# Kernel optimization log

Measured on AMD Instinct MI355X. Metric: run time of the kernel, lower is better.

The kernel has to match this reference:

```python
import jax, jax.numpy as jnp
import numpy as np

N = 50000
IN_C = 128
HID = 64
HEADS = 4
OUT_C = 64
E_RAND = 800000
NEG_SLOPE = 0.2  # PyG GATConv default


def setup_inputs() -> dict:
    key = jax.random.key(0)
    ks = jax.random.split(key, 10)
    x = jax.random.normal(ks[0], (N, IN_C), dtype=jnp.float32)
    src = jax.random.randint(ks[1], (E_RAND,), 0, N)
    dst = jax.random.randint(ks[2], (E_RAND,), 0, N)
    loops = jnp.arange(N)
    # PyG GATConv adds self-loops by default; append them here
    edge_index = jnp.stack([jnp.concatenate([src, loops]),
                            jnp.concatenate([dst, loops])], axis=0).astype(jnp.int64)
    s = 0.05
    W1 = jax.random.normal(ks[3], (IN_C, HEADS * HID), dtype=jnp.float32) * s
    att_src1 = jax.random.normal(ks[4], (HEADS, HID), dtype=jnp.float32) * s
    att_dst1 = jax.random.normal(ks[5], (HEADS, HID), dtype=jnp.float32) * s
    b1 = jnp.zeros((HEADS * HID,), dtype=jnp.float32)
    W2 = jax.random.normal(ks[6], (HEADS * HID, OUT_C), dtype=jnp.float32) * s
    att_src2 = jax.random.normal(ks[7], (1, OUT_C), dtype=jnp.float32) * s
    att_dst2 = jax.random.normal(ks[8], (1, OUT_C), dtype=jnp.float32) * s
    b2 = jnp.zeros((OUT_C,), dtype=jnp.float32)
    return {"x": x, "edge_index": edge_index, "W1": W1, "att_src1": att_src1,
            "att_dst1": att_dst1, "b1": b1, "W2": W2, "att_src2": att_src2,
            "att_dst2": att_dst2, "b2": b2}


def gat_conv(x, src, dst, W, att_src, att_dst, bias, heads, ch, concat):
    n = x.shape[0]
    h = (x @ W).reshape(n, heads, ch)                      # [N,H,C]
    a_src = jnp.einsum('nhc,hc->nh', h, att_src)           # [N,H]
    a_dst = jnp.einsum('nhc,hc->nh', h, att_dst)
    e = jax.nn.leaky_relu(a_src[src] + a_dst[dst], NEG_SLOPE)  # [E,H]
    # segment softmax over incoming edges of each dst node
    m = jax.ops.segment_max(e, dst, num_segments=n)
    ex = jnp.exp(e - m[dst])
    ssum = jax.ops.segment_sum(ex, dst, num_segments=n)
    alpha = ex / jnp.where(ssum[dst] > 0, ssum[dst], 1.0)  # [E,H]
    msg = h[src] * alpha[:, :, None]                        # [E,H,C]
    out = jax.ops.segment_sum(msg, dst, num_segments=n)     # [N,H,C]
    out = out.reshape(n, heads * ch) if concat else out.mean(axis=1)
    return out + bias


def reference(x, edge_index, W1, att_src1, att_dst1, b1, W2, att_src2, att_dst2, b2):
    src, dst = edge_index[0], edge_index[1]
    # eval mode: feature dropout and attention dropout are identity
    h = gat_conv(x, src, dst, W1, att_src1, att_dst1, b1, HEADS, HID, True)
    h = jax.nn.elu(h)
    out = gat_conv(h, src, dst, W2, att_src2, att_dst2, b2, 1, OUT_C, False)
    return out
```

## Files before the change

kernel.cpp:

```cpp
#include <hip/hip_runtime.h>
#include <hip/hip_bf16.h>

#define IN_C 128
#define HID 64
#define HEADS 4
#define OUT_C 64
#define NEG_SLOPE 0.2f

typedef __attribute__((ext_vector_type(8))) short bfrag8;
typedef __attribute__((ext_vector_type(4))) float facc4;

__device__ __forceinline__ float bf16u_to_f(unsigned short u) {
  return __uint_as_float(((unsigned)u) << 16);
}
__device__ __forceinline__ float lof(unsigned u) {
  return __uint_as_float(u << 16);
}
__device__ __forceinline__ float hif(unsigned u) {
  return __uint_as_float(u & 0xffff0000u);
}
__device__ __forceinline__ unsigned short f_to_bf16u(float f) {
  return __bfloat16_as_ushort(__float2bfloat16(f));
}
__device__ __forceinline__ float leaky(float x) {
  return (x > 0.f) ? x : NEG_SLOPE * x;
}

__global__ __launch_bounds__(256) void cvt_w_kernel(
    const float* __restrict__ W1, const float* __restrict__ W2,
    unsigned short* __restrict__ B1img, unsigned short* __restrict__ B2img) {
  int i = blockIdx.x * 256 + threadIdx.x;
  if (i < 4096) {
    int g = i & 7, n = (i >> 3) & 255, kt = i >> 11;
    unsigned short q[8];
#pragma unroll
    for (int e = 0; e < 8; ++e)
      q[e] = f_to_bf16u(W1[(size_t)(kt * 64 + g * 8 + e) * 256 + n]);
    *reinterpret_cast<uint4*>(&B1img[kt * 16384 + n * 64 + ((g ^ (n & 7)) << 3)]) =
        *reinterpret_cast<const uint4*>(q);
  } else if (i < 4096 + 2048) {
    int j = i - 4096;
    int g = j & 7, n = (j >> 3) & 63, kt = j >> 9;
    unsigned short q[8];
#pragma unroll
    for (int e = 0; e < 8; ++e)
      q[e] = f_to_bf16u(W2[(size_t)(kt * 64 + g * 8 + e) * 64 + n]);
    *reinterpret_cast<uint4*>(&B2img[kt * 4096 + n * 64 + ((g ^ (n & 7)) << 3)]) =
        *reinterpret_cast<const uint4*>(q);
  }
}

__global__ __launch_bounds__(256) void mfma_gemm1_wide(
    const float* __restrict__ A, const unsigned short* __restrict__ B1img,
    const float* __restrict__ att_src, const float* __restrict__ att_dst,
    unsigned short* __restrict__ Hout, float* __restrict__ a_src,
    float* __restrict__ a_dst, int M) {
  __shared__ unsigned short As[64 * 64];
  __shared__ unsigned short Bs[256 * 64];
  const int t = threadIdx.x;
  const int wid = t >> 6, lane = t & 63;
  const int lg = lane >> 4, li = lane & 15;
  const int bm = blockIdx.x * 64;

  facc4 acc[16];
#pragma unroll
  for (int fn = 0; fn < 16; ++fn) acc[fn] = (facc4)(0.f);

#pragma unroll
  for (int kt = 0; kt < 2; ++kt) {
#pragma unroll
    for (int p = 0; p < 2; ++p) {
      int flat = t + p * 256;
      int row = flat >> 3, g = flat & 7;
      int gr = bm + row;
      float4 v0 = make_float4(0.f, 0.f, 0.f, 0.f), v1 = v0;
      if (gr < M) {
        const float* src = &A[(size_t)gr * 128 + kt * 64 + g * 8];
        v0 = *reinterpret_cast<const float4*>(src);
        v1 = *reinterpret_cast<const float4*>(src + 4);
      }
      unsigned short q[8];
      q[0] = f_to_bf16u(v0.x); q[1] = f_to_bf16u(v0.y);
      q[2] = f_to_bf16u(v0.z); q[3] = f_to_bf16u(v0.w);
      q[4] = f_to_bf16u(v1.x); q[5] = f_to_bf16u(v1.y);
      q[6] = f_to_bf16u(v1.z); q[7] = f_to_bf16u(v1.w);
      *reinterpret_cast<uint4*>(&As[row * 64 + ((g ^ (row & 7)) << 3)]) =
          *reinterpret_cast<const uint4*>(q);
    }
#pragma unroll
    for (int p = 0; p < 8; ++p) {
      int gi = t + p * 256;
      *reinterpret_cast<uint4*>(&Bs[gi * 8]) =
          *reinterpret_cast<const uint4*>(&B1img[kt * 16384 + gi * 8]);
    }
    __syncthreads();
#pragma unroll
    for (int ks = 0; ks < 2; ++ks) {
      int arow = wid * 16 + li;
      int gk = ks * 4 + lg;
      bfrag8 a = *reinterpret_cast<const bfrag8*>(
          &As[arow * 64 + ((gk ^ (arow & 7)) << 3)]);
#pragma unroll
      for (int fn = 0; fn < 16; ++fn) {
        int col = fn * 16 + li;
        bfrag8 b = *reinterpret_cast<const bfrag8*>(
            &Bs[col * 64 + ((gk ^ (col & 7)) << 3)]);
        acc[fn] =
            __builtin_amdgcn_mfma_f32_16x16x32_bf16(a, b, acc[fn], 0, 0, 0);
      }
    }
    __syncthreads();
  }

#pragma unroll
  for (int reg = 0; reg < 4; ++reg) {
    int row = bm + wid * 16 + lg * 4 + reg;
    if (row < M) {
#pragma unroll
      for (int fn = 0; fn < 16; ++fn)
        Hout[(size_t)row * 256 + fn * 16 + li] = f_to_bf16u(acc[fn][reg]);
    }
#pragma unroll
    for (int h = 0; h < 4; ++h) {
      float ps = 0.f, pd = 0.f;
#pragma unroll
      for (int q = 0; q < 4; ++q) {
        int fn = h * 4 + q;
        float c = acc[fn][reg];
        ps += c * att_src[fn * 16 + li];
        pd += c * att_dst[fn * 16 + li];
      }
#pragma unroll
      for (int m = 1; m < 16; m <<= 1) {
        ps += __shfl_xor(ps, m);
        pd += __shfl_xor(pd, m);
      }
      if (row < M && li == 0) {
        a_src[(size_t)row * 4 + h] = ps;
        a_dst[(size_t)row * 4 + h] = pd;
      }
    }
  }
}

__global__ __launch_bounds__(256) void mfma_gemm2(
    const unsigned short* __restrict__ A, const unsigned short* __restrict__ B2img,
    const float* __restrict__ att_src, const float* __restrict__ att_dst,
    unsigned short* __restrict__ Hout, float* __restrict__ a_src,
    float* __restrict__ a_dst, int M) {
  __shared__ unsigned short As[64 * 64];
  __shared__ unsigned short Bs[64 * 64];
  const int t = threadIdx.x;
  const int wid = t >> 6, lane = t & 63;
  const int lg = lane >> 4, li = lane & 15;
  const int bm = blockIdx.x * 64;

  facc4 acc[4];
#pragma unroll
  for (int fn = 0; fn < 4; ++fn) acc[fn] = (facc4)(0.f);

#pragma unroll
  for (int kt = 0; kt < 4; ++kt) {
#pragma unroll
    for (int p = 0; p < 2; ++p) {
      int flat = t + p * 256;
      int row = flat >> 3, g = flat & 7;
      int gr = bm + row;
      uint4 v = make_uint4(0, 0, 0, 0);
      if (gr < M)
        v = *reinterpret_cast<const uint4*>(&A[(size_t)gr * 256 + kt * 64 + g * 8]);
      *reinterpret_cast<uint4*>(&As[row * 64 + ((g ^ (row & 7)) << 3)]) = v;
    }
#pragma unroll
    for (int p = 0; p < 2; ++p) {
      int gi = t + p * 256;
      *reinterpret_cast<uint4*>(&Bs[gi * 8]) =
          *reinterpret_cast<const uint4*>(&B2img[kt * 4096 + gi * 8]);
    }
    __syncthreads();
#pragma unroll
    for (int ks = 0; ks < 2; ++ks) {
      int arow = wid * 16 + li;
      int gk = ks * 4 + lg;
      bfrag8 a = *reinterpret_cast<const bfrag8*>(
          &As[arow * 64 + ((gk ^ (arow & 7)) << 3)]);
#pragma unroll
      for (int fn = 0; fn < 4; ++fn) {
        int col = fn * 16 + li;
        bfrag8 b = *reinterpret_cast<const bfrag8*>(
            &Bs[col * 64 + ((gk ^ (col & 7)) << 3)]);
        acc[fn] =
            __builtin_amdgcn_mfma_f32_16x16x32_bf16(a, b, acc[fn], 0, 0, 0);
      }
    }
    __syncthreads();
  }

  float s_att[4], d_att[4];
#pragma unroll
  for (int fn = 0; fn < 4; ++fn) {
    s_att[fn] = att_src[fn * 16 + li];
    d_att[fn] = att_dst[fn * 16 + li];
  }
#pragma unroll
  for (int reg = 0; reg < 4; ++reg) {
    int row = bm + wid * 16 + lg * 4 + reg;
    float ps = 0.f, pd = 0.f;
#pragma unroll
    for (int fn = 0; fn < 4; ++fn) {
      float c = acc[fn][reg];
      ps += c * s_att[fn];
      pd += c * d_att[fn];
    }
#pragma unroll
    for (int m = 1; m < 16; m <<= 1) {
      ps += __shfl_xor(ps, m);
      pd += __shfl_xor(pd, m);
    }
    if (row < M) {
#pragma unroll
      for (int fn = 0; fn < 4; ++fn)
        Hout[(size_t)row * 64 + fn * 16 + li] = f_to_bf16u(acc[fn][reg]);
      if (li == 0) {
        a_src[row] = ps;
        a_dst[row] = pd;
      }
    }
  }
}

__global__ void hist_rank_kernel(const int* __restrict__ dst, int E,
                                 int* __restrict__ deg, int* __restrict__ rank) {
  int e = blockIdx.x * blockDim.x + threadIdx.x;
  if (e < E) rank[e] = atomicAdd(&deg[dst[e]], 1);
}

__device__ __forceinline__ int pad4(int d) { return (d + 3) & ~3; }

__global__ __launch_bounds__(256) void scan_partial_kernel(
    const int* __restrict__ deg, int n, int* __restrict__ partials) {
  __shared__ int sm[256];
  int t = threadIdx.x;
  int i = blockIdx.x * 256 + t;
  sm[t] = (i < n) ? pad4(deg[i]) : 0;
  __syncthreads();
  for (int off = 128; off > 0; off >>= 1) {
    if (t < off) sm[t] += sm[t + off];
    __syncthreads();
  }
  if (t == 0) partials[blockIdx.x] = sm[0];
}

__global__ __launch_bounds__(256) void scan_expand_kernel(
    const int* __restrict__ deg, int n, const int* __restrict__ partials,
    int nb, int* __restrict__ offsets, int* __restrict__ ssrc) {
  __shared__ int smp[256];
  __shared__ int sm[256];
  int t = threadIdx.x;
  smp[t] = (t < nb) ? partials[t] : 0;
  __syncthreads();
  for (int off = 1; off < 256; off <<= 1) {
    int u = (t >= off) ? smp[t - off] : 0;
    __syncthreads();
    smp[t] += u;
    __syncthreads();
  }
  int base = (blockIdx.x > 0) ? smp[blockIdx.x - 1] : 0;
  int i = blockIdx.x * 256 + t;
  int d = (i < n) ? deg[i] : 0;
  int v = pad4(d);
  sm[t] = v;
  __syncthreads();
  for (int off = 1; off < 256; off <<= 1) {
    int u = (t >= off) ? sm[t - off] : 0;
    __syncthreads();
    sm[t] += u;
    __syncthreads();
  }
  int excl = sm[t] - v + base;
  if (i < n) {
    offsets[i] = excl;
    for (int k = d; k < v; ++k) ssrc[excl + k] = -1;
  }
}

__global__ void scatter_kernel(const int* __restrict__ src,
                               const int* __restrict__ dst,
                               const int* __restrict__ rank,
                               const int* __restrict__ offsets, int E,
                               int* __restrict__ ssrc) {
  int e = blockIdx.x * blockDim.x + threadIdx.x;
  if (e < E) ssrc[offsets[dst[e]] + rank[e]] = src[e];
}

__global__ __launch_bounds__(256) void agg1_kernel(
    const unsigned short* __restrict__ h1, const float* __restrict__ as1,
    const float* __restrict__ ad1, const int* __restrict__ ssrc,
    const int* __restrict__ offsets, const int* __restrict__ deg,
    const float* __restrict__ bias, unsigned short* __restrict__ out,
    int n_nodes) {
  int wave = (int)((blockIdx.x * blockDim.x + threadIdx.x) >> 6);
  int lane = threadIdx.x & 63;
  if (wave >= n_nodes) return;
  int head = lane >> 4;
  int off = offsets[wave];
  int cnt = deg[wave];
  int last = ((cnt + 3) >> 2) - 1;
  const int* S_ = ssrc + off;
  float ad = ad1[wave * 4 + head];
  const int pbase = lane & 48;

  auto ldS = [&](int g) {
    return *reinterpret_cast<const int4*>(S_ + min(g, last) * 4);
  };
  auto gK = [&](int4 S, float* a_out) {
    int sk = (lane & 1) ? S.y : S.x;
    int sk2 = (lane & 1) ? S.w : S.z;
    sk = (lane & 2) ? sk2 : sk;
    *a_out = as1[max(sk, 0) * 4 + head];
    return sk;
  };
  auto mkP = [&](int sk, float a) {
    float pk = (sk >= 0) ? __expf(leaky(a + ad)) : 0.f;
    return make_float4(__shfl(pk, pbase), __shfl(pk, pbase + 1),
                       __shfl(pk, pbase + 2), __shfl(pk, pbase + 3));
  };
  auto gat = [&](int s) {
    return *reinterpret_cast<const uint2*>(
        &h1[(size_t)max(s, 0) * 256 + lane * 4]);
  };

  float l = 0.f, a0 = 0.f, a1 = 0.f, a2 = 0.f, a3 = 0.f;

  int4 Sg0 = ldS(0), Sg1 = ldS(1);
  int4 SgP = ldS(2);
  uint2 HA0 = gat(Sg0.x), HA1 = gat(Sg0.y), HA2 = gat(Sg0.z), HA3 = gat(Sg0.w);
  uint2 HB0 = gat(Sg1.x), HB1 = gat(Sg1.y), HB2 = gat(Sg1.z), HB3 = gat(Sg1.w);
  float aKA, aKB;
  int skA = gK(Sg0, &aKA);
  int skB = gK(Sg1, &aKB);
  float4 PA = mkP(skA, aKA), PB;

  int j = 0;
  auto step = [&](float4& Pc, float4& Pn, uint2& Hc0, uint2& Hc1, uint2& Hc2,
                  uint2& Hc3, int& skN, float& aKN, int skC, float aKC) {
    Pn = mkP(skC, aKC);
    skN = gK(SgP, &aKN);
    l += Pc.x + Pc.y + Pc.z + Pc.w;
    a0 += Pc.x * lof(Hc0.x) + Pc.y * lof(Hc1.x) + Pc.z * lof(Hc2.x) +
          Pc.w * lof(Hc3.x);
    a1 += Pc.x * hif(Hc0.x) + Pc.y * hif(Hc1.x) + Pc.z * hif(Hc2.x) +
          Pc.w * hif(Hc3.x);
    a2 += Pc.x * lof(Hc0.y) + Pc.y * lof(Hc1.y) + Pc.z * lof(Hc2.y) +
          Pc.w * lof(Hc3.y);
    a3 += Pc.x * hif(Hc0.y) + Pc.y * hif(Hc1.y) + Pc.z * hif(Hc2.y) +
          Pc.w * hif(Hc3.y);
    Hc0 = gat(SgP.x); Hc1 = gat(SgP.y); Hc2 = gat(SgP.z); Hc3 = gat(SgP.w);
    SgP = ldS(j + 3);
  };

  for (;;) {
    step(PA, PB, HA0, HA1, HA2, HA3, skA, aKA, skB, aKB);
    if (++j > last) break;
    step(PB, PA, HB0, HB1, HB2, HB3, skB, aKB, skA, aKA);
    if (++j > last) break;
  }

  float inv = 1.0f / l;
  int col = lane * 4;
  float4 b4 = *reinterpret_cast<const float4*>(&bias[col]);
  float o0 = a0 * inv + b4.x;
  float o1 = a1 * inv + b4.y;
  float o2 = a2 * inv + b4.z;
  float o3 = a3 * inv + b4.w;
  o0 = o0 > 0.f ? o0 : __expf(o0) - 1.f;
  o1 = o1 > 0.f ? o1 : __expf(o1) - 1.f;
  o2 = o2 > 0.f ? o2 : __expf(o2) - 1.f;
  o3 = o3 > 0.f ? o3 : __expf(o3) - 1.f;
  unsigned short q[4];
  q[0] = f_to_bf16u(o0); q[1] = f_to_bf16u(o1);
  q[2] = f_to_bf16u(o2); q[3] = f_to_bf16u(o3);
  *reinterpret_cast<ushort4*>(&out[(size_t)wave * 256 + col]) =
      *reinterpret_cast<const ushort4*>(q);
}

__global__ __launch_bounds__(256) void agg2_kernel(
    const unsigned short* __restrict__ h2, const float* __restrict__ as2,
    const float* __restrict__ ad2, const int* __restrict__ ssrc,
    const int* __restrict__ offsets, const int* __restrict__ deg,
    const float* __restrict__ bias, float* __restrict__ out, int n_nodes) {
  int wave = (int)((blockIdx.x * blockDim.x + threadIdx.x) >> 6);
  int lane = threadIdx.x & 63;
  if (wave >= n_nodes) return;
  int off = offsets[wave];
  int cnt = deg[wave];
  int last = ((cnt + 3) >> 2) - 1;
  const int* S_ = ssrc + off;
  float ad = ad2[wave];

  auto ldS = [&](int g) {
    return *reinterpret_cast<const int4*>(S_ + min(g, last) * 4);
  };
  auto gK = [&](int4 S, float* a_out) {
    int sk = (lane & 1) ? S.y : S.x;
    int sk2 = (lane & 1) ? S.w : S.z;
    sk = (lane & 2) ? sk2 : sk;
    *a_out = as2[max(sk, 0)];
    return sk;
  };
  auto mkP = [&](int sk, float a) {
    float pk = (sk >= 0) ? __expf(leaky(a + ad)) : 0.f;
    return make_float4(__shfl(pk, 0), __shfl(pk, 1), __shfl(pk, 2),
                       __shfl(pk, 3));
  };
  auto gat = [&](int s) { return h2[(size_t)max(s, 0) * 64 + lane]; };

  float l = 0.f, acc = 0.f;

  int4 Sg0 = ldS(0), Sg1 = ldS(1);
  int4 SgP = ldS(2);
  unsigned short HA0 = gat(Sg0.x), HA1 = gat(Sg0.y), HA2 = gat(Sg0.z),
                 HA3 = gat(Sg0.w);
  unsigned short HB0 = gat(Sg1.x), HB1 = gat(Sg1.y), HB2 = gat(Sg1.z),
                 HB3 = gat(Sg1.w);
  float aKA, aKB;
  int skA = gK(Sg0, &aKA);
  int skB = gK(Sg1, &aKB);
  float4 PA = mkP(skA, aKA), PB;

  int j = 0;
  auto step = [&](float4& Pc, float4& Pn, unsigned short& Hc0,
                  unsigned short& Hc1, unsigned short& Hc2, unsigned short& Hc3,
                  int& skN, float& aKN, int skC, float aKC) {
    Pn = mkP(skC, aKC);
    skN = gK(SgP, &aKN);
    l += Pc.x + Pc.y + Pc.z + Pc.w;
    acc += Pc.x * bf16u_to_f(Hc0) + Pc.y * bf16u_to_f(Hc1) +
           Pc.z * bf16u_to_f(Hc2) + Pc.w * bf16u_to_f(Hc3);
    Hc0 = gat(SgP.x); Hc1 = gat(SgP.y); Hc2 = gat(SgP.z); Hc3 = gat(SgP.w);
    SgP = ldS(j + 3);
  };

  for (;;) {
    step(PA, PB, HA0, HA1, HA2, HA3, skA, aKA, skB, aKB);
    if (++j > last) break;
    step(PB, PA, HB0, HB1, HB2, HB3, skB, aKB, skA, aKA);
    if (++j > last) break;
  }

  out[(size_t)wave * 64 + lane] = acc / l + bias[lane];
}

extern "C" void kernel_launch(void* const* d_in, const int* in_sizes, int n_in,
                              void* d_out, int out_size, void* d_ws,
                              size_t ws_size, hipStream_t stream) {
  const float* x = (const float*)d_in[0];
  const int* edge_index = (const int*)d_in[1];
  const float* W1 = (const float*)d_in[2];
  const float* att_src1 = (const float*)d_in[3];
  const float* att_dst1 = (const float*)d_in[4];
  const float* b1 = (const float*)d_in[5];
  const float* W2 = (const float*)d_in[6];
  const float* att_src2 = (const float*)d_in[7];
  const float* att_dst2 = (const float*)d_in[8];
  const float* b2 = (const float*)d_in[9];

  const int n = in_sizes[0] / IN_C;
  const int E = in_sizes[1] / 2;
  const int* src = edge_index;
  const int* dst = edge_index + E;
  const int nb = (n + 255) / 256;
  const int stride = (E + 4 * n + 3) & ~3;

  char* ws = (char*)d_ws;
  size_t off = 0;
  auto carve = [&](size_t bytes) -> void* {
    void* p = ws + off;
    off = (off + bytes + 255) & ~(size_t)255;
    return p;
  };
  unsigned short* h1b = (unsigned short*)carve((size_t)n * 256 * 2);
  unsigned short* hact = (unsigned short*)carve((size_t)n * 256 * 2);
  unsigned short* h2b = (unsigned short*)carve((size_t)n * 64 * 2);
  unsigned short* B1img = (unsigned short*)carve(32768 * 2);
  unsigned short* B2img = (unsigned short*)carve(16384 * 2);
  float* as1 = (float*)carve((size_t)n * 4 * 4);
  float* ad1 = (float*)carve((size_t)n * 4 * 4);
  float* as2 = (float*)carve((size_t)n * 4);
  float* ad2 = (float*)carve((size_t)n * 4);
  int* deg = (int*)carve((size_t)n * 4);
  int* offsets = (int*)carve((size_t)n * 4);
  int* rank = (int*)carve((size_t)E * 4);
  int* ssrc = (int*)carve((size_t)stride * 4);
  int* partials = (int*)carve((size_t)nb * 4);

  hipMemsetAsync(deg, 0, (size_t)n * 4, stream);

  cvt_w_kernel<<<24, 256, 0, stream>>>(W1, W2, B1img, B2img);
  mfma_gemm1_wide<<<(n + 63) / 64, 256, 0, stream>>>(
      x, B1img, att_src1, att_dst1, h1b, as1, ad1, n);
  hist_rank_kernel<<<(E + 255) / 256, 256, 0, stream>>>(dst, E, deg, rank);
  scan_partial_kernel<<<nb, 256, 0, stream>>>(deg, n, partials);
  scan_expand_kernel<<<nb, 256, 0, stream>>>(deg, n, partials, nb, offsets,
                                             ssrc);
  scatter_kernel<<<(E + 255) / 256, 256, 0, stream>>>(src, dst, rank, offsets,
                                                      E, ssrc);
  agg1_kernel<<<(n * 64 + 255) / 256, 256, 0, stream>>>(
      h1b, as1, ad1, ssrc, offsets, deg, b1, hact, n);
  mfma_gemm2<<<(n + 63) / 64, 256, 0, stream>>>(hact, B2img, att_src2,
                                                att_dst2, h2b, as2, ad2, n);
  agg2_kernel<<<(n * 64 + 255) / 256, 256, 0, stream>>>(
      h2b, as2, ad2, ssrc, offsets, deg, b2, (float*)d_out, n);
}
```

Measured before the change: 273.3 us.

## Fuse deg memset into weight setup, histogram into GEMM1, vectorize scatter

Folds the deg memset into the weight-conversion kernel. It also moves the dst histogram/rank atomics into extra blocks of the first GEMM launch, so histogram work overlaps with the GEMM and two launches disappear. The histogram and scatter kernels now handle four edges per thread using int4 loads. In exchange, the histogram blocks inherit the GEMM kernel's large static shared-memory footprint, which may limit their occupancy. The scatter grid also assumes the edge count is close to a multiple of four.

```diff
diff --git a/kernel.cpp b/kernel.cpp
--- a/kernel.cpp
+++ b/kernel.cpp
@@ -26,38 +26,67 @@
   return (x > 0.f) ? x : NEG_SLOPE * x;
 }
 
-__global__ __launch_bounds__(256) void cvt_w_kernel(
+__global__ __launch_bounds__(256) void setup_kernel(
     const float* __restrict__ W1, const float* __restrict__ W2,
-    unsigned short* __restrict__ B1img, unsigned short* __restrict__ B2img) {
-  int i = blockIdx.x * 256 + threadIdx.x;
-  if (i < 4096) {
-    int g = i & 7, n = (i >> 3) & 255, kt = i >> 11;
-    unsigned short q[8];
-#pragma unroll
-    for (int e = 0; e < 8; ++e)
-      q[e] = f_to_bf16u(W1[(size_t)(kt * 64 + g * 8 + e) * 256 + n]);
-    *reinterpret_cast<uint4*>(&B1img[kt * 16384 + n * 64 + ((g ^ (n & 7)) << 3)]) =
-        *reinterpret_cast<const uint4*>(q);
-  } else if (i < 4096 + 2048) {
-    int j = i - 4096;
-    int g = j & 7, n = (j >> 3) & 63, kt = j >> 9;
-    unsigned short q[8];
-#pragma unroll
-    for (int e = 0; e < 8; ++e)
-      q[e] = f_to_bf16u(W2[(size_t)(kt * 64 + g * 8 + e) * 64 + n]);
-    *reinterpret_cast<uint4*>(&B2img[kt * 4096 + n * 64 + ((g ^ (n & 7)) << 3)]) =
-        *reinterpret_cast<const uint4*>(q);
-  }
-}
-
-__global__ __launch_bounds__(256) void mfma_gemm1_wide(
+    unsigned short* __restrict__ B1img, unsigned short* __restrict__ B2img,
+    int* __restrict__ deg, int n) {
+  int bid = blockIdx.x;
+  if (bid < 24) {
+    int i = bid * 256 + threadIdx.x;
+    if (i < 4096) {
+      int g = i & 7, nn = (i >> 3) & 255, kt = i >> 11;
+      unsigned short q[8];
+#pragma unroll
+      for (int e = 0; e < 8; ++e)
+        q[e] = f_to_bf16u(W1[(size_t)(kt * 64 + g * 8 + e) * 256 + nn]);
+      *reinterpret_cast<uint4*>(
+          &B1img[kt * 16384 + nn * 64 + ((g ^ (nn & 7)) << 3)]) =
+          *reinterpret_cast<const uint4*>(q);
+    } else if (i < 4096 + 2048) {
+      int j = i - 4096;
+      int g = j & 7, nn = (j >> 3) & 63, kt = j >> 9;
+      unsigned short q[8];
+#pragma unroll
+      for (int e = 0; e < 8; ++e)
+        q[e] = f_to_bf16u(W2[(size_t)(kt * 64 + g * 8 + e) * 64 + nn]);
+      *reinterpret_cast<uint4*>(
+          &B2img[kt * 4096 + nn * 64 + ((g ^ (nn & 7)) << 3)]) =
+          *reinterpret_cast<const uint4*>(q);
+    }
+  } else {
+    int i = (bid - 24) * 1024 + threadIdx.x * 4;
+    if (i < n)
+      *reinterpret_cast<int4*>(&deg[i]) = make_int4(0, 0, 0, 0);
+  }
+}
+
+__global__ __launch_bounds__(256) void gemm1_hist_kernel(
     const float* __restrict__ A, const unsigned short* __restrict__ B1img,
     const float* __restrict__ att_src, const float* __restrict__ att_dst,
     unsigned short* __restrict__ Hout, float* __restrict__ a_src,
-    float* __restrict__ a_dst, int M) {
+    float* __restrict__ a_dst, int M, int G1,
+    const int* __restrict__ dst, int E, int* __restrict__ deg,
+    int* __restrict__ rank) {
   __shared__ unsigned short As[64 * 64];
   __shared__ unsigned short Bs[256 * 64];
   const int t = threadIdx.x;
+
+  if ((int)blockIdx.x >= G1) {
+    int e0 = ((int)blockIdx.x - G1) * 1024 + t * 4;
+    if (e0 + 3 < E) {
+      int4 d4 = *reinterpret_cast<const int4*>(&dst[e0]);
+      int4 r4;
+      r4.x = atomicAdd(&deg[d4.x], 1);
+      r4.y = atomicAdd(&deg[d4.y], 1);
+      r4.z = atomicAdd(&deg[d4.z], 1);
+      r4.w = atomicAdd(&deg[d4.w], 1);
+      *reinterpret_cast<int4*>(&rank[e0]) = r4;
+    } else {
+      for (int e = e0; e < E; ++e) rank[e] = atomicAdd(&deg[dst[e]], 1);
+    }
+    return;
+  }
+
   const int wid = t >> 6, lane = t & 63;
   const int lg = lane >> 4, li = lane & 15;
   const int bm = blockIdx.x * 64;
@@ -229,12 +258,6 @@
   }
 }
 
-__global__ void hist_rank_kernel(const int* __restrict__ dst, int E,
-                                 int* __restrict__ deg, int* __restrict__ rank) {
-  int e = blockIdx.x * blockDim.x + threadIdx.x;
-  if (e < E) rank[e] = atomicAdd(&deg[dst[e]], 1);
-}
-
 __device__ __forceinline__ int pad4(int d) { return (d + 3) & ~3; }
 
 __global__ __launch_bounds__(256) void scan_partial_kernel(
@@ -289,8 +312,18 @@
                                const int* __restrict__ rank,
                                const int* __restrict__ offsets, int E,
                                int* __restrict__ ssrc) {
-  int e = blockIdx.x * blockDim.x + threadIdx.x;
-  if (e < E) ssrc[offsets[dst[e]] + rank[e]] = src[e];
+  int e0 = (blockIdx.x * blockDim.x + threadIdx.x) * 4;
+  if (e0 + 3 < E) {
+    int4 s4 = *reinterpret_cast<const int4*>(&src[e0]);
+    int4 d4 = *reinterpret_cast<const int4*>(&dst[e0]);
+    int4 r4 = *reinterpret_cast<const int4*>(&rank[e0]);
+    ssrc[offsets[d4.x] + r4.x] = s4.x;
+    ssrc[offsets[d4.y] + r4.y] = s4.y;
+    ssrc[offsets[d4.z] + r4.z] = s4.z;
+    ssrc[offsets[d4.w] + r4.w] = s4.w;
+  } else {
+    for (int e = e0; e < E; ++e) ssrc[offsets[dst[e]] + rank[e]] = src[e];
+  }
 }
 
 __global__ __launch_bounds__(256) void agg1_kernel(
@@ -494,17 +527,21 @@
   int* ssrc = (int*)carve((size_t)stride * 4);
   int* partials = (int*)carve((size_t)nb * 4);
 
-  hipMemsetAsync(deg, 0, (size_t)n * 4, stream);
-
-  cvt_w_kernel<<<24, 256, 0, stream>>>(W1, W2, B1img, B2img);
-  mfma_gemm1_wide<<<(n + 63) / 64, 256, 0, stream>>>(
-      x, B1img, att_src1, att_dst1, h1b, as1, ad1, n);
-  hist_rank_kernel<<<(E + 255) / 256, 256, 0, stream>>>(dst, E, deg, rank);
+  {
+    int zb = (n + 1023) / 1024;
+    setup_kernel<<<24 + zb, 256, 0, stream>>>(W1, W2, B1img, B2img, deg, n);
+  }
+  {
+    int G1 = (n + 63) / 64;
+    int H = (E + 1023) / 1024;
+    gemm1_hist_kernel<<<G1 + H, 256, 0, stream>>>(
+        x, B1img, att_src1, att_dst1, h1b, as1, ad1, n, G1, dst, E, deg, rank);
+  }
   scan_partial_kernel<<<nb, 256, 0, stream>>>(deg, n, partials);
   scan_expand_kernel<<<nb, 256, 0, stream>>>(deg, n, partials, nb, offsets,
                                              ssrc);
-  scatter_kernel<<<(E + 255) / 256, 256, 0, stream>>>(src, dst, rank, offsets,
-                                                      E, ssrc);
+  scatter_kernel<<<(E / 4 + 255) / 256, 256, 0, stream>>>(src, dst, rank,
+                                                          offsets, E, ssrc);
   agg1_kernel<<<(n * 64 + 255) / 256, 256, 0, stream>>>(
       h1b, as1, ad1, ssrc, offsets, deg, b1, hact, n);
   mfma_gemm2<<<(n + 63) / 64, 256, 0, stream>>>(hact, B2img, att_src2,
```

Result: no change. 270.2 us (-1.1%).
